# Optimization experiments

Measured on AMD Instinct MI355X. Metric: run time of the kernel, lower is better.

The kernel has to match this reference:

```python
import jax, jax.numpy as jnp
import numpy as np

B, T, D, H = 2, 2048, 1024, 16
Dh = D // H
V = 32000  # vocab for kWTA potentials
KW_DECAY, KW_THR, K_WIN = 0.7, 1.0, 5
GAIN_UP, GAIN_DOWN = 1.5, 0.6
SPIKE_THR = 0.5


def setup_inputs() -> dict:
    key = jax.random.key(0)
    ks = jax.random.split(key, 10)
    x = jax.random.normal(ks[0], (B, T, D), dtype=jnp.float32)
    token_ids = jax.random.randint(ks[1], (B, T), 0, V)
    # xavier_uniform with gain 0.5 for square DxD weights
    bound = 0.5 * np.sqrt(6.0 / (D + D))
    def w(k):
        return jax.random.uniform(k, (D, D), dtype=jnp.float32, minval=-bound, maxval=bound)
    Wr, Wk, Wv, Wo = w(ks[2]), w(ks[3]), w(ks[4]), w(ks[5])
    bo = jnp.zeros((D,), dtype=jnp.float32)
    def tm(k):
        return jax.random.uniform(k, (1, 1, D), dtype=jnp.float32, minval=0.1, maxval=0.9)
    time_mix_k, time_mix_v, time_mix_r = tm(ks[6]), tm(ks[7]), tm(ks[8])
    return {"x": x, "token_ids": token_ids, "Wr": Wr, "Wk": Wk, "Wv": Wv,
            "Wo": Wo, "bo": bo, "time_mix_k": time_mix_k,
            "time_mix_v": time_mix_v, "time_mix_r": time_mix_r}


def kwta_gains(token_ids):
    """Sequential spiking k-WTA over the flattened token stream -> (V,) gains."""
    ids = token_ids.reshape(-1)
    def step(carry, tid):
        pot, spk = carry
        pot = pot * KW_DECAY
        pot = pot.at[tid].add(1.0)          # bincount of single token
        fired = pot >= KW_THR
        spk = spk + fired.astype(jnp.int32)
        pot = jnp.where(fired, pot - KW_THR, pot)  # soft reset
        return (pot, spk), None
    init = (jnp.zeros((V,), jnp.float32), jnp.zeros((V,), jnp.int32))
    (pot, spk), _ = jax.lax.scan(step, init, ids)
    values = spk.astype(jnp.float32) * 1e6 + pot
    topk_idx = jax.lax.top_k(values, K_WIN)[1]
    gains = jnp.where(spk > 0, GAIN_DOWN, 1.0).astype(jnp.float32)
    gains = gains.at[topk_idx].set(GAIN_UP)
    return gains


def spike_activation(x):
    # training-mode STE: hard spikes forward, clamp(1-|x-thr|,0,1) surrogate grad
    spikes = (x > SPIKE_THR).astype(x.dtype)
    ste = jnp.clip(1.0 - jnp.abs(x - SPIKE_THR), 0.0, 1.0)
    return spikes + ste - jax.lax.stop_gradient(ste)


def reference(x, token_ids, Wr, Wk, Wv, Wo, bo, time_mix_k, time_mix_v, time_mix_r):
    gains = jax.lax.stop_gradient(kwta_gains(token_ids))[:D]  # (D,)
    # token shift: prev_state starts as zeros
    prev_x = jnp.concatenate([jnp.zeros((B, 1, D), x.dtype), x[:, :-1]], axis=1)
    def mix(tm):
        m = tm.reshape(D) * gains               # adaptive time mixing with kWTA gains
        return m * x + (1.0 - m) * prev_x
    xr, xk, xv = mix(time_mix_r), mix(time_mix_k), mix(time_mix_v)
    r = xr @ Wr.T                                # [B,T,D]
    k = spike_activation(xk @ Wk.T)
    v = xv @ Wv.T
    def heads(t):
        return t.reshape(B, T, H, Dh).transpose(0, 2, 1, 3)  # [B,H,T,Dh]
    q_, k_, v_ = heads(r), heads(k), heads(v)
    # chunked_attention is an exact tiled full (non-causal) softmax attention
    scores = jnp.einsum('bhqd,bhkd->bhqk', q_, k_) * (1.0 / np.sqrt(Dh))
    attn = jax.nn.softmax(scores, axis=-1)
    out = jnp.einsum('bhqk,bhkd->bhqd', attn, v_)
    out = out.transpose(0, 2, 1, 3).reshape(B, T, D)
    out = jax.nn.sigmoid(r) * out                # receptance gating
    return out @ Wo.T + bo
```

## Files before the change

### kernel.cpp

```cpp
#include <hip/hip_runtime.h>
#include <stdint.h>

static constexpr int CB = 2, CT = 2048, CD = 1024, CH = 16, CDh = 64, CV = 32000;
static constexpr int CM = CB * CT;

typedef float f32x4 __attribute__((ext_vector_type(4)));
typedef float f32x16 __attribute__((ext_vector_type(16)));
typedef short s16x8 __attribute__((ext_vector_type(8)));

__device__ __forceinline__ unsigned short f2bf(float f) {
  unsigned u = __builtin_bit_cast(unsigned, f);
  unsigned r = 0x7FFFu + ((u >> 16) & 1u);
  return (unsigned short)((u + r) >> 16);
}
__device__ __forceinline__ float bf2f(unsigned short h) {
  unsigned u = ((unsigned)h) << 16;
  return __builtin_bit_cast(float, u);
}
__device__ __forceinline__ unsigned pkrh(float a, float b) {
  unsigned ua = __builtin_bit_cast(unsigned, a) + 0x8000u;
  unsigned ub = __builtin_bit_cast(unsigned, b) + 0x8000u;
  return __builtin_amdgcn_perm(ub, ua, 0x07060302);
}
__device__ __forceinline__ void lds_cp16(const void* g, void* l) {
  __builtin_amdgcn_global_load_lds(
      (const __attribute__((address_space(1))) unsigned*)g,
      (__attribute__((address_space(3))) unsigned*)l, 16, 0, 0);
}

__global__ void nsr_bincount(const int* __restrict__ ids, int* __restrict__ bins) {
  int i = blockIdx.x * 256 + threadIdx.x;
  if (i < CM) atomicAdd(&bins[ids[i]], 1);
}

__device__ __forceinline__ void chain5(unsigned n, unsigned& b0, unsigned& b1, unsigned& b2,
                                       unsigned& b3, unsigned& b4) {
  unsigned t;
  t = b0 > n ? b0 : n; n = b0 > n ? n : b0; b0 = t;
  t = b1 > n ? b1 : n; n = b1 > n ? n : b1; b1 = t;
  t = b2 > n ? b2 : n; n = b2 > n ? n : b2; b2 = t;
  t = b3 > n ? b3 : n; n = b3 > n ? n : b3; b3 = t;
  b4 = b4 > n ? b4 : n;
}

__global__ void nsr_gains(const int* __restrict__ bins, float* __restrict__ gains) {
  __shared__ unsigned l5[1280];
  __shared__ unsigned w5[320];
  __shared__ unsigned m5[80];
  __shared__ unsigned fin[5];
  int tid = threadIdx.x;
  unsigned b0 = 0, b1 = 0, b2 = 0, b3 = 0, b4 = 0;
  for (int i = tid; i < CV; i += 256) {
    unsigned key = (((unsigned)bins[i]) << 15) | (unsigned)(32767 - i);
    chain5(key, b0, b1, b2, b3, b4);
  }
  l5[tid] = b0; l5[256 + tid] = b1; l5[512 + tid] = b2; l5[768 + tid] = b3; l5[1024 + tid] = b4;
  __syncthreads();
  if (tid < 64) {
    unsigned c0 = 0, c1 = 0, c2 = 0, c3 = 0, c4 = 0;
    for (int i = tid; i < 1280; i += 64) chain5(l5[i], c0, c1, c2, c3, c4);
    w5[tid] = c0; w5[64 + tid] = c1; w5[128 + tid] = c2; w5[192 + tid] = c3; w5[256 + tid] = c4;
  }
  __syncthreads();
  if (tid < 16) {
    unsigned c0 = 0, c1 = 0, c2 = 0, c3 = 0, c4 = 0;
    for (int i = tid; i < 320; i += 16) chain5(w5[i], c0, c1, c2, c3, c4);
    m5[tid] = c0; m5[16 + tid] = c1; m5[32 + tid] = c2; m5[48 + tid] = c3; m5[64 + tid] = c4;
  }
  __syncthreads();
  if (tid == 0) {
    unsigned c0 = 0, c1 = 0, c2 = 0, c3 = 0, c4 = 0;
    for (int i = 0; i < 80; ++i) chain5(m5[i], c0, c1, c2, c3, c4);
    fin[0] = c0; fin[1] = c1; fin[2] = c2; fin[3] = c3; fin[4] = c4;
  }
  __syncthreads();
  for (int i = tid; i < CD; i += 256) {
    int cnt = bins[i];
    float g = cnt > 0 ? 0.6f : 1.0f;
    unsigned key = (((unsigned)cnt) << 15) | (unsigned)(32767 - i);
    if (key == fin[0] || key == fin[1] || key == fin[2] || key == fin[3] || key == fin[4])
      g = 1.5f;
    gains[i] = g;
  }
}

__device__ __forceinline__ unsigned short mix1(float tm, float g, float xc, float px) {
  float m = tm * g;
  return f2bf(m * xc + (1.f - m) * px);
}

__global__ void nsr_cvtw_mix(const float* __restrict__ Wr, const float* __restrict__ Wk,
                             const float* __restrict__ Wv, const float* __restrict__ Wo,
                             unsigned short* __restrict__ dst, const float* __restrict__ x,
                             const float* __restrict__ gains, const float* __restrict__ tmr,
                             const float* __restrict__ tmk, const float* __restrict__ tmv,
                             unsigned short* __restrict__ xr, unsigned short* __restrict__ xk,
                             unsigned short* __restrict__ xv) {
  int bid = blockIdx.x;
  if (bid < 4096) {
    int i = bid * 256 + threadIdx.x;
    int which = i >> 18;
    int j = (i & 0x3FFFF) << 2;
    const float* s = which == 0 ? Wr : which == 1 ? Wk : which == 2 ? Wv : Wo;
    float4 v = *(const float4*)(s + j);
    ushort4 o = make_ushort4(f2bf(v.x), f2bf(v.y), f2bf(v.z), f2bf(v.w));
    *(ushort4*)(dst + (size_t)which * (CD * CD) + j) = o;
  } else {
    int i = (bid - 4096) * 256 + threadIdx.x;
    int m = i >> 8;
    int d = (i & 255) << 2;
    int t = m & (CT - 1);
    size_t base = (size_t)m * CD + d;
    float4 xc = *(const float4*)(x + base);
    float4 px = make_float4(0.f, 0.f, 0.f, 0.f);
    if (t > 0) px = *(const float4*)(x + base - CD);
    float4 g = *(const float4*)(gains + d);
    float4 ar = *(const float4*)(tmr + d);
    float4 ak = *(const float4*)(tmk + d);
    float4 av = *(const float4*)(tmv + d);
    *(ushort4*)(xr + base) = make_ushort4(mix1(ar.x, g.x, xc.x, px.x), mix1(ar.y, g.y, xc.y, px.y),
                                          mix1(ar.z, g.z, xc.z, px.z), mix1(ar.w, g.w, xc.w, px.w));
    *(ushort4*)(xk + base) = make_ushort4(mix1(ak.x, g.x, xc.x, px.x), mix1(ak.y, g.y, xc.y, px.y),
                                          mix1(ak.z, g.z, xc.z, px.z), mix1(ak.w, g.w, xc.w, px.w));
    *(ushort4*)(xv + base) = make_ushort4(mix1(av.x, g.x, xc.x, px.x), mix1(av.y, g.y, xc.y, px.y),
                                          mix1(av.z, g.z, xc.z, px.z), mix1(av.w, g.w, xc.w, px.w));
  }
}

__device__ __forceinline__ void gemm128(const unsigned short* __restrict__ A,
                                        const unsigned short* __restrict__ W, int m0, int n0,
                                        int K, int tid, f32x4 acc[4][4],
                                        unsigned short* As, unsigned short* Bs) {
  const f32x4 fz = {0.f, 0.f, 0.f, 0.f};
  int lane = tid & 63, w = tid >> 6;
  int wm = (w >> 1) << 6, wn = (w & 1) << 6;
  int l15 = lane & 15, quad = lane >> 4;
#pragma unroll
  for (int mt = 0; mt < 4; ++mt)
#pragma unroll
    for (int nt = 0; nt < 4; ++nt) acc[mt][nt] = fz;
  for (int k0 = 0; k0 < K; k0 += 32) {
#pragma unroll
    for (int i = 0; i < 2; ++i) {
      int chunk = i * 256 + tid;
      int r = chunk >> 2, cp = chunk & 3, c = cp ^ (r & 3);
      lds_cp16(A + (size_t)(m0 + r) * K + k0 + c * 8, &As[(chunk & ~63) << 3]);
      lds_cp16(W + (size_t)(n0 + r) * K + k0 + c * 8, &Bs[(chunk & ~63) << 3]);
    }
    __syncthreads();
    s16x8 af[4], bf[4];
#pragma unroll
    for (int mt = 0; mt < 4; ++mt) {
      int row = wm + mt * 16 + l15;
      af[mt] = *(const s16x8*)&As[row * 32 + ((quad ^ (row & 3)) << 3)];
    }
#pragma unroll
    for (int nt = 0; nt < 4; ++nt) {
      int row = wn + nt * 16 + l15;
      bf[nt] = *(const s16x8*)&Bs[row * 32 + ((quad ^ (row & 3)) << 3)];
    }
#pragma unroll
    for (int mt = 0; mt < 4; ++mt)
#pragma unroll
      for (int nt = 0; nt < 4; ++nt)
        acc[mt][nt] = __builtin_amdgcn_mfma_f32_16x16x32_bf16(af[mt], bf[nt], acc[mt][nt], 0, 0, 0);
    __syncthreads();
  }
}

__global__ __launch_bounds__(256) void nsr_proj(const unsigned short* __restrict__ xr,
                                                const unsigned short* __restrict__ xk,
                                                const unsigned short* __restrict__ xv,
                                                const unsigned short* __restrict__ Wb,
                                                unsigned short* __restrict__ r,
                                                unsigned short* __restrict__ k,
                                                unsigned short* __restrict__ v) {
  __shared__ alignas(16) unsigned short As[128 * 32];
  __shared__ alignas(16) unsigned short Bs[128 * 32];
  int bid = blockIdx.x;
  int which = bid >> 8;
  int bl = bid & 255;
  int m0 = (bl >> 3) << 7, n0 = (bl & 7) << 7;
  const unsigned short* A = which == 0 ? xr : which == 1 ? xk : xv;
  const unsigned short* W = Wb + (size_t)which * (CD * CD);
  f32x4 acc[4][4];
  gemm128(A, W, m0, n0, CD, threadIdx.x, acc, As, Bs);
  unsigned short* out = which == 0 ? r : which == 1 ? k : v;
  int lane = threadIdx.x & 63, w = threadIdx.x >> 6;
  int wm = (w >> 1) << 6, wn = (w & 1) << 6;
  int l15 = lane & 15, quad = lane >> 4;
#pragma unroll
  for (int mt = 0; mt < 4; ++mt)
#pragma unroll
    for (int nt = 0; nt < 4; ++nt)
#pragma unroll
      for (int rr = 0; rr < 4; ++rr) {
        int grow = m0 + wm + mt * 16 + quad * 4 + rr;
        int gcol = n0 + wn + nt * 16 + l15;
        float val = acc[mt][nt][rr];
        if (which == 1) val = val > 0.5f ? 1.0f : 0.0f;
        out[(size_t)grow * CD + gcol] = f2bf(val);
      }
}

__global__ void nsr_vtrans(const unsigned short* __restrict__ v, unsigned short* __restrict__ vt) {
  __shared__ alignas(16) unsigned short tile[64][72];
  int bid = blockIdx.x;
  int rt = bid >> 4, h = bid & 15;
  int m0 = rt << 6;
  int tid = threadIdx.x;
  int row = tid >> 2, cc = (tid & 3) << 4;
  const s16x8* src = (const s16x8*)(v + (size_t)(m0 + row) * CD + (h << 6) + cc);
  *(s16x8*)&tile[row][cc] = src[0];
  *(s16x8*)&tile[row][cc + 8] = src[1];
  __syncthreads();
  int b = m0 >> 11;
  int t0 = (m0 & (CT - 1));
  int dl = tid >> 2;
  int tcc = (tid & 3) << 4;
  unsigned short tmp[16];
#pragma unroll
  for (int j = 0; j < 16; ++j) tmp[j] = tile[tcc + j][dl];
  size_t obase = ((size_t)((b * CH + h) * CDh + dl)) * CT + t0 + tcc;
  *(s16x8*)(vt + obase) = *(s16x8*)&tmp[0];
  *(s16x8*)(vt + obase + 8) = *(s16x8*)&tmp[8];
}

__global__ __launch_bounds__(512, 4) void nsr_attn(const unsigned short* __restrict__ rbf,
                                                   const unsigned short* __restrict__ kbf,
                                                   const unsigned short* __restrict__ vt,
                                                   unsigned short* __restrict__ gated) {
  __shared__ alignas(16) unsigned char smem[32768];
  __shared__ float denp[2][128];
  unsigned short* Ks = (unsigned short*)smem;
  unsigned short* Vs = (unsigned short*)(smem + 16384);
  float* Ored = (float*)smem;

  const f32x16 fz16 = {0.f, 0.f, 0.f, 0.f, 0.f, 0.f, 0.f, 0.f,
                       0.f, 0.f, 0.f, 0.f, 0.f, 0.f, 0.f, 0.f};
  const float EXSC = 0.125f * 1.44269504088896f;
  int bid = blockIdx.x;
  int b = bid & 1, hd = (bid >> 1) & 15, qt = bid >> 5;
  int tid = threadIdx.x, lane = tid & 63, w = tid >> 6;
  int l31 = lane & 31, hbit = lane >> 5;
  int qh = w & 3, kq2 = w >> 2;

  const unsigned short* qrow = rbf + (size_t)(b * CT + qt * 128 + qh * 32 + l31) * CD + hd * 64;
  s16x8 qfrag[4];
#pragma unroll
  for (int s4 = 0; s4 < 4; ++s4) qfrag[s4] = *(const s16x8*)(qrow + s4 * 16 + hbit * 8);

  const unsigned short* kgbase = kbf + (size_t)(b * CT) * CD + hd * 64;
  const unsigned short* vgbase = vt + (size_t)((b * CH + hd) * CDh) * CT;

  f32x16 o_acc[2];
  o_acc[0] = fz16;
  o_acc[1] = fz16;
  float den = 0.f;

  for (int kt = 0; kt < 16; ++kt) {
#pragma unroll
    for (int i = 0; i < 2; ++i) {
      int L = i * 512 + tid;
      int key = L >> 3, cp = L & 7, c = cp ^ (key & 7);
      lds_cp16(kgbase + (size_t)(kt * 128 + key) * CD + c * 8, &Ks[(L & ~63) << 3]);
      int d = L >> 4, cp2 = L & 15, c2 = (cp2 & 8) | ((cp2 ^ d) & 7);
      lds_cp16(vgbase + (size_t)d * CT + kt * 128 + c2 * 8, &Vs[(L & ~63) << 3]);
    }
    __syncthreads();

#pragma unroll
    for (int ktile = 0; ktile < 2; ++ktile) {
      int keyrow = kq2 * 64 + ktile * 32 + l31;
      f32x16 sc = fz16;
#pragma unroll
      for (int s4 = 0; s4 < 4; ++s4) {
        int c = s4 * 2 + hbit;
        int cp = c ^ (keyrow & 7);
        s16x8 af = *(const s16x8*)&Ks[keyrow * 64 + cp * 8];
        sc = __builtin_amdgcn_mfma_f32_32x32x16_bf16(af, qfrag[s4], sc, 0, 0, 0);
      }
      float pexp[16];
#pragma unroll
      for (int rr = 0; rr < 16; ++rr) {
        float p = __builtin_amdgcn_exp2f(sc[rr] * EXSC);
        pexp[rr] = p;
        den += p;
      }
#pragma unroll
      for (int s = 0; s < 2; ++s) {
        int rb = 8 * s;
        unsigned P01 = pkrh(pexp[rb + 0], pexp[rb + 1]);
        unsigned P23 = pkrh(pexp[rb + 2], pexp[rb + 3]);
        unsigned P45 = pkrh(pexp[rb + 4], pexp[rb + 5]);
        unsigned P67 = pkrh(pexp[rb + 6], pexp[rb + 7]);
        unsigned send0 = hbit ? P01 : P45;
        unsigned send1 = hbit ? P23 : P67;
        unsigned recv0 = (unsigned)__shfl_xor((int)send0, 32);
        unsigned recv1 = (unsigned)__shfl_xor((int)send1, 32);
        unsigned br[4];
        br[0] = hbit ? recv0 : P01;
        br[1] = hbit ? recv1 : P23;
        br[2] = hbit ? P45 : recv0;
        br[3] = hbit ? P67 : recv1;
        s16x8 bfrag = __builtin_bit_cast(s16x8, *(const unsigned(*)[4])br);
#pragma unroll
        for (int dt = 0; dt < 2; ++dt) {
          int drow = dt * 32 + l31;
          int c = kq2 * 8 + ktile * 4 + s * 2 + hbit;
          int cp = (c & 8) | ((c ^ drow) & 7);
          s16x8 vf = *(const s16x8*)&Vs[drow * 128 + cp * 8];
          o_acc[dt] = __builtin_amdgcn_mfma_f32_32x32x16_bf16(vf, bfrag, o_acc[dt], 0, 0, 0);
        }
      }
    }
    __syncthreads();
  }

  den += __shfl_xor(den, 32);
  if (hbit == 0) denp[kq2][qh * 32 + l31] = den;
  __syncthreads();
  float rinv = 1.0f / (denp[0][qh * 32 + l31] + denp[1][qh * 32 + l31]);

  if (kq2 == 1) {
#pragma unroll
    for (int dt = 0; dt < 2; ++dt)
#pragma unroll
      for (int rr = 0; rr < 16; ++rr) {
        int d = dt * 32 + (rr & 3) + 8 * (rr >> 2) + 4 * hbit;
        Ored[qh * 2048 + d * 32 + l31] = o_acc[dt][rr];
      }
  }
  __syncthreads();
  if (kq2 == 0) {
#pragma unroll
    for (int dt = 0; dt < 2; ++dt)
#pragma unroll
      for (int rr = 0; rr < 16; ++rr) {
        int d = dt * 32 + (rr & 3) + 8 * (rr >> 2) + 4 * hbit;
        int idx = qh * 2048 + d * 32 + l31;
        Ored[idx] = (o_acc[dt][rr] + Ored[idx]) * rinv;
      }
  }
  __syncthreads();

  int q = tid >> 2, dc = tid & 3;
  size_t grow = (size_t)(b * CT + qt * 128 + q) * CD + hd * 64 + dc * 16;
  s16x8 rv0 = *(const s16x8*)(rbf + grow);
  s16x8 rv1 = *(const s16x8*)(rbf + grow + 8);
  unsigned short outv[16];
#pragma unroll
  for (int i = 0; i < 16; ++i) {
    float o = Ored[(q >> 5) * 2048 + (dc * 16 + i) * 32 + (q & 31)];
    float rv = bf2f(i < 8 ? ((unsigned short*)&rv0)[i] : ((unsigned short*)&rv1)[i - 8]);
    float sig = 1.f / (1.f + __expf(-rv));
    outv[i] = f2bf(sig * o);
  }
  *(s16x8*)(gated + grow) = *(s16x8*)&outv[0];
  *(s16x8*)(gated + grow + 8) = *(s16x8*)&outv[8];
}

__global__ __launch_bounds__(256) void nsr_out(const unsigned short* __restrict__ gated,
                                               const unsigned short* __restrict__ Wo,
                                               const float* __restrict__ bo,
                                               float* __restrict__ out) {
  __shared__ alignas(16) unsigned short As[128 * 32];
  __shared__ alignas(16) unsigned short Bs[128 * 32];
  int bl = blockIdx.x;
  int m0 = (bl >> 3) << 7, n0 = (bl & 7) << 7;
  f32x4 acc[4][4];
  gemm128(gated, Wo, m0, n0, CD, threadIdx.x, acc, As, Bs);
  int lane = threadIdx.x & 63, w = threadIdx.x >> 6;
  int wm = (w >> 1) << 6, wn = (w & 1) << 6;
  int l15 = lane & 15, quad = lane >> 4;
#pragma unroll
  for (int mt = 0; mt < 4; ++mt)
#pragma unroll
    for (int nt = 0; nt < 4; ++nt)
#pragma unroll
      for (int rr = 0; rr < 4; ++rr) {
        int grow = m0 + wm + mt * 16 + quad * 4 + rr;
        int gcol = n0 + wn + nt * 16 + l15;
        out[(size_t)grow * CD + gcol] = acc[mt][nt][rr] + bo[gcol];
      }
}

extern "C" void kernel_launch(void* const* d_in, const int* in_sizes, int n_in,
                              void* d_out, int out_size, void* d_ws, size_t ws_size,
                              hipStream_t stream) {
  const float* x = (const float*)d_in[0];
  const int* ids = (const int*)d_in[1];
  const float* Wr = (const float*)d_in[2];
  const float* Wk = (const float*)d_in[3];
  const float* Wv = (const float*)d_in[4];
  const float* Wo = (const float*)d_in[5];
  const float* bo = (const float*)d_in[6];
  const float* tmk = (const float*)d_in[7];
  const float* tmv = (const float*)d_in[8];
  const float* tmr = (const float*)d_in[9];

  char* ws = (char*)d_ws;
  size_t off = 0;
  int* bins = (int*)(ws + off); off += 131072;
  float* gains = (float*)(ws + off); off += 4096;
  unsigned short* Wb = (unsigned short*)(ws + off); off += (size_t)4 * CD * CD * 2;
  unsigned short* xr = (unsigned short*)(ws + off); off += (size_t)CM * CD * 2;
  unsigned short* xk = (unsigned short*)(ws + off); off += (size_t)CM * CD * 2;
  unsigned short* xv = (unsigned short*)(ws + off); off += (size_t)CM * CD * 2;
  unsigned short* rb = (unsigned short*)(ws + off); off += (size_t)CM * CD * 2;
  unsigned short* kb = (unsigned short*)(ws + off); off += (size_t)CM * CD * 2;
  unsigned short* vb = (unsigned short*)(ws + off); off += (size_t)CM * CD * 2;
  unsigned short* vtb = (unsigned short*)(ws + off); off += (size_t)CM * CD * 2;
  unsigned short* gatedb = (unsigned short*)(ws + off); off += (size_t)CM * CD * 2;

  hipMemsetAsync(bins, 0, CV * sizeof(int), stream);
  nsr_bincount<<<16, 256, 0, stream>>>(ids, bins);
  nsr_gains<<<1, 256, 0, stream>>>(bins, gains);
  nsr_cvtw_mix<<<8192, 256, 0, stream>>>(Wr, Wk, Wv, Wo, Wb, x, gains, tmr, tmk, tmv, xr, xk, xv);
  nsr_proj<<<768, 256, 0, stream>>>(xr, xk, xv, Wb, rb, kb, vb);
  nsr_vtrans<<<1024, 256, 0, stream>>>(vb, vtb);
  nsr_attn<<<512, 512, 0, stream>>>(rb, kb, vtb, gatedb);
  nsr_out<<<256, 256, 0, stream>>>(gatedb, Wb + (size_t)3 * CD * CD, bo, (float*)d_out);
}
```

Before: 255.3 us.

## Fuse bincount into gains, fuse V transpose into projection, streamline attention loop

Merges the bincount kernel into a single 1024-thread gains kernel and removes one reduction stage. The V projection now writes its transposed per-head layout straight from registers through an LDS tile, which drops the separate transpose kernel and the intermediate V buffer. In attention, the softmax scale is folded into Q up front, LDS and global pointers are precomputed outside the loop, and the denominator is split into two accumulators. Risks are the larger LDS footprint in nsr_proj, which may reduce occupancy for all projection blocks, and slightly different rounding from pre-scaling Q in bf16.

```diff
diff --git a/kernel.cpp b/kernel.cpp
--- a/kernel.cpp
+++ b/kernel.cpp
@@ -26,11 +26,6 @@
   __builtin_amdgcn_global_load_lds(
       (const __attribute__((address_space(1))) unsigned*)g,
       (__attribute__((address_space(3))) unsigned*)l, 16, 0, 0);
-}
-
-__global__ void nsr_bincount(const int* __restrict__ ids, int* __restrict__ bins) {
-  int i = blockIdx.x * 256 + threadIdx.x;
-  if (i < CM) atomicAdd(&bins[ids[i]], 1);
 }
 
 __device__ __forceinline__ void chain5(unsigned n, unsigned& b0, unsigned& b1, unsigned& b2,
@@ -43,44 +38,42 @@
   b4 = b4 > n ? b4 : n;
 }
 
-__global__ void nsr_gains(const int* __restrict__ bins, float* __restrict__ gains) {
-  __shared__ unsigned l5[1280];
+__global__ __launch_bounds__(1024) void nsr_gains(const int* __restrict__ ids,
+                                                  int* __restrict__ bins,
+                                                  float* __restrict__ gains) {
+  __shared__ unsigned l5[5120];
   __shared__ unsigned w5[320];
-  __shared__ unsigned m5[80];
   __shared__ unsigned fin[5];
   int tid = threadIdx.x;
+#pragma unroll
+  for (int i = 0; i < 4; ++i) atomicAdd(&bins[ids[i * 1024 + tid]], 1);
+  __syncthreads();
   unsigned b0 = 0, b1 = 0, b2 = 0, b3 = 0, b4 = 0;
-  for (int i = tid; i < CV; i += 256) {
+  for (int i = tid; i < CV; i += 1024) {
     unsigned key = (((unsigned)bins[i]) << 15) | (unsigned)(32767 - i);
     chain5(key, b0, b1, b2, b3, b4);
   }
-  l5[tid] = b0; l5[256 + tid] = b1; l5[512 + tid] = b2; l5[768 + tid] = b3; l5[1024 + tid] = b4;
+  l5[tid] = b0; l5[1024 + tid] = b1; l5[2048 + tid] = b2; l5[3072 + tid] = b3; l5[4096 + tid] = b4;
   __syncthreads();
   if (tid < 64) {
     unsigned c0 = 0, c1 = 0, c2 = 0, c3 = 0, c4 = 0;
-    for (int i = tid; i < 1280; i += 64) chain5(l5[i], c0, c1, c2, c3, c4);
+    for (int i = tid; i < 5120; i += 64) chain5(l5[i], c0, c1, c2, c3, c4);
     w5[tid] = c0; w5[64 + tid] = c1; w5[128 + tid] = c2; w5[192 + tid] = c3; w5[256 + tid] = c4;
-  }
-  __syncthreads();
-  if (tid < 16) {
-    unsigned c0 = 0, c1 = 0, c2 = 0, c3 = 0, c4 = 0;
-    for (int i = tid; i < 320; i += 16) chain5(w5[i], c0, c1, c2, c3, c4);
-    m5[tid] = c0; m5[16 + tid] = c1; m5[32 + tid] = c2; m5[48 + tid] = c3; m5[64 + tid] = c4;
   }
   __syncthreads();
   if (tid == 0) {
     unsigned c0 = 0, c1 = 0, c2 = 0, c3 = 0, c4 = 0;
-    for (int i = 0; i < 80; ++i) chain5(m5[i], c0, c1, c2, c3, c4);
+    for (int i = 0; i < 320; ++i) chain5(w5[i], c0, c1, c2, c3, c4);
     fin[0] = c0; fin[1] = c1; fin[2] = c2; fin[3] = c3; fin[4] = c4;
   }
   __syncthreads();
-  for (int i = tid; i < CD; i += 256) {
-    int cnt = bins[i];
+  {
+    int cnt = bins[tid];
     float g = cnt > 0 ? 0.6f : 1.0f;
-    unsigned key = (((unsigned)cnt) << 15) | (unsigned)(32767 - i);
+    unsigned key = (((unsigned)cnt) << 15) | (unsigned)(32767 - tid);
     if (key == fin[0] || key == fin[1] || key == fin[2] || key == fin[3] || key == fin[4])
       g = 1.5f;
-    gains[i] = g;
+    gains[tid] = g;
   }
 }
 
@@ -174,9 +167,10 @@
                                                 const unsigned short* __restrict__ Wb,
                                                 unsigned short* __restrict__ r,
                                                 unsigned short* __restrict__ k,
-                                                unsigned short* __restrict__ v) {
+                                                unsigned short* __restrict__ vt) {
   __shared__ alignas(16) unsigned short As[128 * 32];
   __shared__ alignas(16) unsigned short Bs[128 * 32];
+  __shared__ alignas(16) unsigned short vts[128 * 136];
   int bid = blockIdx.x;
   int which = bid >> 8;
   int bl = bid & 255;
@@ -185,45 +179,48 @@
   const unsigned short* W = Wb + (size_t)which * (CD * CD);
   f32x4 acc[4][4];
   gemm128(A, W, m0, n0, CD, threadIdx.x, acc, As, Bs);
-  unsigned short* out = which == 0 ? r : which == 1 ? k : v;
-  int lane = threadIdx.x & 63, w = threadIdx.x >> 6;
+  int tid = threadIdx.x;
+  int lane = tid & 63, w = tid >> 6;
   int wm = (w >> 1) << 6, wn = (w & 1) << 6;
   int l15 = lane & 15, quad = lane >> 4;
-#pragma unroll
-  for (int mt = 0; mt < 4; ++mt)
-#pragma unroll
-    for (int nt = 0; nt < 4; ++nt)
-#pragma unroll
-      for (int rr = 0; rr < 4; ++rr) {
-        int grow = m0 + wm + mt * 16 + quad * 4 + rr;
-        int gcol = n0 + wn + nt * 16 + l15;
-        float val = acc[mt][nt][rr];
-        if (which == 1) val = val > 0.5f ? 1.0f : 0.0f;
-        out[(size_t)grow * CD + gcol] = f2bf(val);
-      }
-}
-
-__global__ void nsr_vtrans(const unsigned short* __restrict__ v, unsigned short* __restrict__ vt) {
-  __shared__ alignas(16) unsigned short tile[64][72];
-  int bid = blockIdx.x;
-  int rt = bid >> 4, h = bid & 15;
-  int m0 = rt << 6;
-  int tid = threadIdx.x;
-  int row = tid >> 2, cc = (tid & 3) << 4;
-  const s16x8* src = (const s16x8*)(v + (size_t)(m0 + row) * CD + (h << 6) + cc);
-  *(s16x8*)&tile[row][cc] = src[0];
-  *(s16x8*)&tile[row][cc + 8] = src[1];
-  __syncthreads();
-  int b = m0 >> 11;
-  int t0 = (m0 & (CT - 1));
-  int dl = tid >> 2;
-  int tcc = (tid & 3) << 4;
-  unsigned short tmp[16];
-#pragma unroll
-  for (int j = 0; j < 16; ++j) tmp[j] = tile[tcc + j][dl];
-  size_t obase = ((size_t)((b * CH + h) * CDh + dl)) * CT + t0 + tcc;
-  *(s16x8*)(vt + obase) = *(s16x8*)&tmp[0];
-  *(s16x8*)(vt + obase + 8) = *(s16x8*)&tmp[8];
+  if (which < 2) {
+    unsigned short* out = which == 0 ? r : k;
+#pragma unroll
+    for (int mt = 0; mt < 4; ++mt)
+#pragma unroll
+      for (int nt = 0; nt < 4; ++nt)
+#pragma unroll
+        for (int rr = 0; rr < 4; ++rr) {
+          int grow = m0 + wm + mt * 16 + quad * 4 + rr;
+          int gcol = n0 + wn + nt * 16 + l15;
+          float val = acc[mt][nt][rr];
+          if (which == 1) val = val > 0.5f ? 1.0f : 0.0f;
+          out[(size_t)grow * CD + gcol] = f2bf(val);
+        }
+  } else {
+#pragma unroll
+    for (int mt = 0; mt < 4; ++mt)
+#pragma unroll
+      for (int nt = 0; nt < 4; ++nt) {
+        int gcl = wn + nt * 16 + l15;
+        int gr = wm + mt * 16 + quad * 4;
+        unsigned lo = pkrh(acc[mt][nt][0], acc[mt][nt][1]);
+        unsigned hi = pkrh(acc[mt][nt][2], acc[mt][nt][3]);
+        uint2 pk = make_uint2(lo, hi);
+        *(uint2*)&vts[gcl * 136 + gr] = pk;
+      }
+    __syncthreads();
+    int b2 = m0 >> 11, t0 = m0 & (CT - 1);
+    int ch = tid & 15, dl2 = tid >> 4;
+#pragma unroll
+    for (int rr2 = 0; rr2 < 8; ++rr2) {
+      int dloc = rr2 * 16 + dl2;
+      int h = (n0 + dloc) >> 6, dl = (n0 + dloc) & 63;
+      s16x8 val = *(const s16x8*)&vts[dloc * 136 + ch * 8];
+      size_t ob = ((size_t)((b2 * CH + h) * CDh + dl)) * CT + t0 + ch * 8;
+      *(s16x8*)(vt + ob) = val;
+    }
+  }
 }
 
 __global__ __launch_bounds__(512, 4) void nsr_attn(const unsigned short* __restrict__ rbf,
@@ -248,52 +245,97 @@
   const unsigned short* qrow = rbf + (size_t)(b * CT + qt * 128 + qh * 32 + l31) * CD + hd * 64;
   s16x8 qfrag[4];
 #pragma unroll
-  for (int s4 = 0; s4 < 4; ++s4) qfrag[s4] = *(const s16x8*)(qrow + s4 * 16 + hbit * 8);
-
-  const unsigned short* kgbase = kbf + (size_t)(b * CT) * CD + hd * 64;
-  const unsigned short* vgbase = vt + (size_t)((b * CH + hd) * CDh) * CT;
+  for (int s4 = 0; s4 < 4; ++s4) {
+    s16x8 qf = *(const s16x8*)(qrow + s4 * 16 + hbit * 8);
+    unsigned* qd = (unsigned*)&qf;
+#pragma unroll
+    for (int j = 0; j < 4; ++j) {
+      float lo = __builtin_bit_cast(float, qd[j] << 16) * EXSC;
+      float hi = __builtin_bit_cast(float, qd[j] & 0xFFFF0000u) * EXSC;
+      qd[j] = pkrh(lo, hi);
+    }
+    qfrag[s4] = qf;
+  }
+
+  const unsigned short* kap[2][4];
+#pragma unroll
+  for (int ktile = 0; ktile < 2; ++ktile) {
+    int keyrow = kq2 * 64 + ktile * 32 + l31;
+#pragma unroll
+    for (int s4 = 0; s4 < 4; ++s4) {
+      int cp = (s4 * 2 + hbit) ^ (keyrow & 7);
+      kap[ktile][s4] = &Ks[keyrow * 64 + cp * 8];
+    }
+  }
+  const unsigned short* vap[2][2][2];
+#pragma unroll
+  for (int ktile = 0; ktile < 2; ++ktile)
+#pragma unroll
+    for (int s = 0; s < 2; ++s)
+#pragma unroll
+      for (int dt = 0; dt < 2; ++dt) {
+        int drow = dt * 32 + l31;
+        int c = kq2 * 8 + ktile * 4 + s * 2 + hbit;
+        int cp = (c & 8) | ((c ^ drow) & 7);
+        vap[ktile][s][dt] = &Vs[drow * 128 + cp * 8];
+      }
+
+  const unsigned short* kgp[2];
+  const unsigned short* vgp[2];
+  unsigned short* ldk[2];
+  unsigned short* ldv[2];
+  {
+    const unsigned short* kgbase = kbf + (size_t)(b * CT) * CD + hd * 64;
+    const unsigned short* vgbase = vt + (size_t)((b * CH + hd) * CDh) * CT;
+#pragma unroll
+    for (int i = 0; i < 2; ++i) {
+      int L = i * 512 + tid;
+      int key = L >> 3, cpk = (L & 7) ^ (key & 7);
+      kgp[i] = kgbase + (size_t)key * CD + cpk * 8;
+      ldk[i] = &Ks[(L & ~63) << 3];
+      int d = L >> 4, cp2 = L & 15, c2 = (cp2 & 8) | ((cp2 ^ d) & 7);
+      vgp[i] = vgbase + (size_t)d * CT + c2 * 8;
+      ldv[i] = &Vs[(L & ~63) << 3];
+    }
+  }
 
   f32x16 o_acc[2];
   o_acc[0] = fz16;
   o_acc[1] = fz16;
-  float den = 0.f;
+  float den0 = 0.f, den1 = 0.f;
 
   for (int kt = 0; kt < 16; ++kt) {
 #pragma unroll
     for (int i = 0; i < 2; ++i) {
-      int L = i * 512 + tid;
-      int key = L >> 3, cp = L & 7, c = cp ^ (key & 7);
-      lds_cp16(kgbase + (size_t)(kt * 128 + key) * CD + c * 8, &Ks[(L & ~63) << 3]);
-      int d = L >> 4, cp2 = L & 15, c2 = (cp2 & 8) | ((cp2 ^ d) & 7);
-      lds_cp16(vgbase + (size_t)d * CT + kt * 128 + c2 * 8, &Vs[(L & ~63) << 3]);
+      lds_cp16(kgp[i], ldk[i]);
+      lds_cp16(vgp[i], ldv[i]);
+      kgp[i] += 128 * CD;
+      vgp[i] += 128;
     }
     __syncthreads();
 
 #pragma unroll
     for (int ktile = 0; ktile < 2; ++ktile) {
-      int keyrow = kq2 * 64 + ktile * 32 + l31;
       f32x16 sc = fz16;
 #pragma unroll
-      for (int s4 = 0; s4 < 4; ++s4) {
-        int c = s4 * 2 + hbit;
-        int cp = c ^ (keyrow & 7);
-        s16x8 af = *(const s16x8*)&Ks[keyrow * 64 + cp * 8];
-        sc = __builtin_amdgcn_mfma_f32_32x32x16_bf16(af, qfrag[s4], sc, 0, 0, 0);
-      }
-      float pexp[16];
-#pragma unroll
-      for (int rr = 0; rr < 16; ++rr) {
-        float p = __builtin_amdgcn_exp2f(sc[rr] * EXSC);
-        pexp[rr] = p;
-        den += p;
-      }
+      for (int s4 = 0; s4 < 4; ++s4)
+        sc = __builtin_amdgcn_mfma_f32_32x32x16_bf16(*(const s16x8*)kap[ktile][s4], qfrag[s4], sc,
+                                                     0, 0, 0);
 #pragma unroll
       for (int s = 0; s < 2; ++s) {
         int rb = 8 * s;
-        unsigned P01 = pkrh(pexp[rb + 0], pexp[rb + 1]);
-        unsigned P23 = pkrh(pexp[rb + 2], pexp[rb + 3]);
-        unsigned P45 = pkrh(pexp[rb + 4], pexp[rb + 5]);
-        unsigned P67 = pkrh(pexp[rb + 6], pexp[rb + 7]);
+        float p0 = __builtin_amdgcn_exp2f(sc[rb + 0]);
+        float p1 = __builtin_amdgcn_exp2f(sc[rb + 1]);
+        float p2 = __builtin_amdgcn_exp2f(sc[rb + 2]);
+        float p3 = __builtin_amdgcn_exp2f(sc[rb + 3]);
+        float p4 = __builtin_amdgcn_exp2f(sc[rb + 4]);
+        float p5 = __builtin_amdgcn_exp2f(sc[rb + 5]);
+        float p6 = __builtin_amdgcn_exp2f(sc[rb + 6]);
+        float p7 = __builtin_amdgcn_exp2f(sc[rb + 7]);
+        den0 += (p0 + p1) + (p2 + p3);
+        den1 += (p4 + p5) + (p6 + p7);
+        unsigned P01 = pkrh(p0, p1), P23 = pkrh(p2, p3);
+        unsigned P45 = pkrh(p4, p5), P67 = pkrh(p6, p7);
         unsigned send0 = hbit ? P01 : P45;
         unsigned send1 = hbit ? P23 : P67;
         unsigned recv0 = (unsigned)__shfl_xor((int)send0, 32);
@@ -304,19 +346,16 @@
         br[2] = hbit ? P45 : recv0;
         br[3] = hbit ? P67 : recv1;
         s16x8 bfrag = __builtin_bit_cast(s16x8, *(const unsigned(*)[4])br);
-#pragma unroll
-        for (int dt = 0; dt < 2; ++dt) {
-          int drow = dt * 32 + l31;
-          int c = kq2 * 8 + ktile * 4 + s * 2 + hbit;
-          int cp = (c & 8) | ((c ^ drow) & 7);
-          s16x8 vf = *(const s16x8*)&Vs[drow * 128 + cp * 8];
-          o_acc[dt] = __builtin_amdgcn_mfma_f32_32x32x16_bf16(vf, bfrag, o_acc[dt], 0, 0, 0);
-        }
+        o_acc[0] = __builtin_amdgcn_mfma_f32_32x32x16_bf16(*(const s16x8*)vap[ktile][s][0], bfrag,
+                                                           o_acc[0], 0, 0, 0);
+        o_acc[1] = __builtin_amdgcn_mfma_f32_32x32x16_bf16(*(const s16x8*)vap[ktile][s][1], bfrag,
+                                                           o_acc[1], 0, 0, 0);
       }
     }
     __syncthreads();
   }
 
+  float den = den0 + den1;
   den += __shfl_xor(den, 32);
   if (hbit == 0) denp[kq2][qh * 32 + l31] = den;
   __syncthreads();
@@ -409,16 +448,13 @@
   unsigned short* xv = (unsigned short*)(ws + off); off += (size_t)CM * CD * 2;
   unsigned short* rb = (unsigned short*)(ws + off); off += (size_t)CM * CD * 2;
   unsigned short* kb = (unsigned short*)(ws + off); off += (size_t)CM * CD * 2;
-  unsigned short* vb = (unsigned short*)(ws + off); off += (size_t)CM * CD * 2;
   unsigned short* vtb = (unsigned short*)(ws + off); off += (size_t)CM * CD * 2;
   unsigned short* gatedb = (unsigned short*)(ws + off); off += (size_t)CM * CD * 2;
 
   hipMemsetAsync(bins, 0, CV * sizeof(int), stream);
-  nsr_bincount<<<16, 256, 0, stream>>>(ids, bins);
-  nsr_gains<<<1, 256, 0, stream>>>(bins, gains);
+  nsr_gains<<<1, 1024, 0, stream>>>(ids, bins, gains);
   nsr_cvtw_mix<<<8192, 256, 0, stream>>>(Wr, Wk, Wv, Wo, Wb, x, gains, tmr, tmk, tmv, xr, xk, xv);
-  nsr_proj<<<768, 256, 0, stream>>>(xr, xk, xv, Wb, rb, kb, vb);
-  nsr_vtrans<<<1024, 256, 0, stream>>>(vb, vtb);
+  nsr_proj<<<768, 256, 0, stream>>>(xr, xk, xv, Wb, rb, kb, vtb);
   nsr_attn<<<512, 512, 0, stream>>>(rb, kb, vtb, gatedb);
   nsr_out<<<256, 256, 0, stream>>>(gatedb, Wb + (size_t)3 * CD * CD, bo, (float*)d_out);
 }
```

Result: faster. 249.6 us (-2.2%).
